# Performance work log

Hardware: AMD Instinct MI355X
Metric: run time of the kernel (lower is better)

## Reference

```python
import jax, jax.numpy as jnp
import numpy as np

N_HEAD = 12

def setup_inputs() -> dict:
    key = jax.random.key(0)
    ks = jax.random.split(key, 5)
    B, T, C = 1, 4096, 768
    scale = 0.02
    return {
        "x": jax.random.normal(ks[0], (B, T, C), jnp.float32),
        "w_attn": jax.random.normal(ks[1], (C, 3 * C), jnp.float32) * scale,
        "b_attn": jax.random.normal(ks[2], (3 * C,), jnp.float32) * scale,
        "w_proj": jax.random.normal(ks[3], (C, C), jnp.float32) * scale,
        "b_proj": jax.random.normal(ks[4], (C,), jnp.float32) * scale,
    }

def reference(x, w_attn, b_attn, w_proj, b_proj):
    B, T, C = x.shape
    H = N_HEAD
    D = C // H
    qkv = x @ w_attn + b_attn                      # [B,T,3C]
    q, k, v = jnp.split(qkv, 3, axis=-1)
    # [B,T,C] -> [B,H,T,D]
    q = q.reshape(B, T, H, D).transpose(0, 2, 1, 3)
    k = k.reshape(B, T, H, D).transpose(0, 2, 1, 3)
    v = v.reshape(B, T, H, D).transpose(0, 2, 1, 3)
    att = jnp.einsum("bhqd,bhkd->bhqk", q, k) * (1.0 / np.sqrt(D))
    causal = jnp.tril(jnp.ones((T, T), bool))
    att = jnp.where(causal[None, None], att, -jnp.inf)
    att = jax.nn.softmax(att, axis=-1)
    y = jnp.einsum("bhqk,bhkd->bhqd", att, v)      # [B,H,T,D]
    y = y.transpose(0, 2, 1, 3).reshape(B, T, C)
    return y @ w_proj + b_proj
```

## Files before the change

### kernel.cpp

```cpp
#include <hip/hip_runtime.h>
#include <hip/hip_bf16.h>
#include <cstdint>
#include <cstddef>

#define NHEAD 12
#define TSEQ  4096
#define CDIM  768

typedef __attribute__((ext_vector_type(8))) short bf16x8;
typedef __attribute__((ext_vector_type(4))) float f32x4;
typedef __attribute__((ext_vector_type(16))) float f32x16;
typedef __attribute__((ext_vector_type(2))) unsigned int u32x2;

typedef __attribute__((address_space(1))) void gvoid;
typedef __attribute__((address_space(3))) void lvoid;

#define QSCALE 0.1803368801111204f

static __device__ __forceinline__ unsigned short f2bf(float f) {
    union { float f; uint32_t u; } v; v.f = f;
    uint32_t u = v.u;
    u += 0x7fffu + ((u >> 16) & 1u);
    return (unsigned short)(u >> 16);
}

static __device__ __forceinline__ f32x4 mfma16(bf16x8 a, bf16x8 b, f32x4 c) {
    return __builtin_amdgcn_mfma_f32_16x16x32_bf16(a, b, c, 0, 0, 0);
}
static __device__ __forceinline__ f32x16 mfma32(bf16x8 a, bf16x8 b, f32x16 c) {
    return __builtin_amdgcn_mfma_f32_32x32x16_bf16(a, b, c, 0, 0, 0);
}
static __device__ __forceinline__ unsigned cvt_pk_bf16(float lo, float hi) {
    unsigned r;
    asm("v_cvt_pk_bf16_f32 %0, %1, %2" : "=v"(r) : "v"(lo), "v"(hi));
    return r;
}


__global__ void cvt_f32_bf16(const float* __restrict__ in, unsigned short* __restrict__ out, int n4) {
    int i = blockIdx.x * blockDim.x + threadIdx.x;
    int stride = gridDim.x * blockDim.x;
    for (int idx = i; idx < n4; idx += stride) {
        float4 v = reinterpret_cast<const float4*>(in)[idx];
        ushort4 o;
        o.x = f2bf(v.x); o.y = f2bf(v.y); o.z = f2bf(v.z); o.w = f2bf(v.w);
        reinterpret_cast<ushort4*>(out)[idx] = o;
    }
}

__global__ void transpose_cvt(const float* __restrict__ W, unsigned short* __restrict__ Wt,
                              int K, int N) {
    __shared__ float tile[32][33];
    int n0 = blockIdx.x * 32;
    int k0 = blockIdx.y * 32;
    int tx = threadIdx.x & 31;
    int ty = threadIdx.x >> 5;
    #pragma unroll
    for (int r = ty; r < 32; r += 8)
        tile[r][tx] = W[(size_t)(k0 + r) * N + n0 + tx];
    __syncthreads();
    #pragma unroll
    for (int r = ty; r < 32; r += 8)
        Wt[(size_t)(n0 + r) * K + k0 + tx] = f2bf(tile[tx][r]);
}


template<int MODE>
__global__ __launch_bounds__(256)
void gemm_bt(const unsigned short* __restrict__ A,
             const unsigned short* __restrict__ Bt,
             const float* __restrict__ bias,
             unsigned short* __restrict__ Qb,
             unsigned short* __restrict__ Kb,
             unsigned short* __restrict__ Vt,
             float* __restrict__ Out,
             int M, int N, int K)
{
    __shared__ __align__(16) unsigned short As[128 * 32];
    __shared__ __align__(16) unsigned short Bs[128 * 32];

    const int tid  = threadIdx.x;
    const int lane = tid & 63;
    const int w    = tid >> 6;
    const int wr   = w >> 1, wc = w & 1;
    const int row0 = blockIdx.x * 128;
    const int col0 = blockIdx.y * 128;
    const int l16  = lane & 15;
    const int lhi  = lane >> 4;

    f32x4 acc[4][4] = {};

    for (int k0 = 0; k0 < K; k0 += 32) {
        __syncthreads();
        #pragma unroll
        for (int r = 0; r < 2; ++r) {
            int b    = r * 4096 + w * 1024 + lane * 16;
            int trow = b >> 6;
            int koff = b & 63;
            const char* gA = (const char*)A  + ((size_t)(row0 + trow) * K + k0) * 2 + koff;
            const char* gB = (const char*)Bt + ((size_t)(col0 + trow) * K + k0) * 2 + koff;
            __builtin_amdgcn_global_load_lds((gvoid*)gA,
                (lvoid*)((char*)As + r * 4096 + w * 1024), 16, 0, 0);
            __builtin_amdgcn_global_load_lds((gvoid*)gB,
                (lvoid*)((char*)Bs + r * 4096 + w * 1024), 16, 0, 0);
        }
        __syncthreads();

        bf16x8 a[4], bfr[4];
        #pragma unroll
        for (int m = 0; m < 4; ++m) {
            int row = wr * 64 + m * 16 + l16;
            a[m] = *reinterpret_cast<const bf16x8*>(&As[row * 32 + lhi * 8]);
        }
        #pragma unroll
        for (int n = 0; n < 4; ++n) {
            int col = wc * 64 + n * 16 + l16;
            bfr[n] = *reinterpret_cast<const bf16x8*>(&Bs[col * 32 + lhi * 8]);
        }
        #pragma unroll
        for (int m = 0; m < 4; ++m)
            #pragma unroll
            for (int n = 0; n < 4; ++n)
                acc[m][n] = mfma16(a[m], bfr[n], acc[m][n]);
    }

    #pragma unroll
    for (int m = 0; m < 4; ++m) {
        int trow = row0 + wr * 64 + m * 16 + lhi * 4;
        #pragma unroll
        for (int n = 0; n < 4; ++n) {
            int ncol = col0 + wc * 64 + n * 16 + l16;
            float bv = bias[ncol];
            #pragma unroll
            for (int j = 0; j < 4; ++j) {
                float v = acc[m][n][j] + bv;
                int t = trow + j;
                if (MODE == 0) {
                    if (ncol < 768) {
                        int hh = ncol >> 6, d = ncol & 63;
                        Qb[((size_t)hh * TSEQ + t) * 64 + d] = f2bf(v * QSCALE);
                    } else if (ncol < 1536) {
                        int c = ncol - 768; int hh = c >> 6, d = c & 63;
                        Kb[((size_t)hh * TSEQ + t) * 64 + d] = f2bf(v);
                    } else {
                        int c = ncol - 1536; int hh = c >> 6, d = c & 63;
                        Vt[((size_t)hh * 64 + d) * TSEQ + t] = f2bf(v);
                    }
                } else {
                    Out[(size_t)t * N + ncol] = v;
                }
            }
        }
    }
}


__global__ __launch_bounds__(64)
void attn_fwd(const unsigned short* __restrict__ Qb,
              const unsigned short* __restrict__ Kb,
              const unsigned short* __restrict__ Vt,
              unsigned short* __restrict__ Y)
{
    const int lane = threadIdx.x & 63;
    const int l31  = lane & 31;
    const int hi   = lane >> 5;
    const int bid  = blockIdx.x;
    const int h    = bid % NHEAD;
    const int qb   = 127 - bid / NHEAD;
    const int q0   = qb * 32;
    const int ntiles = q0 / 64 + 1;

    const unsigned short* Qh = Qb + (size_t)h * TSEQ * 64;
    const unsigned short* Kh = Kb + (size_t)h * TSEQ * 64;
    const unsigned short* Vh = Vt + (size_t)h * 64 * TSEQ;

    bf16x8 qf[4];
    #pragma unroll
    for (int ks = 0; ks < 4; ++ks)
        qf[ks] = *reinterpret_cast<const bf16x8*>(
            &Qh[(size_t)(q0 + l31) * 64 + ks * 16 + hi * 8]);

    f32x16 o0 = {}, o1 = {};
    float mrun = -1e30f, lrun = 0.f;

    bf16x8 kfA[2][4], kfB[2][4];
    #pragma unroll
    for (int sub = 0; sub < 2; ++sub)
        #pragma unroll
        for (int ks = 0; ks < 4; ++ks)
            kfA[sub][ks] = *reinterpret_cast<const bf16x8*>(
                &Kh[(size_t)(sub * 32 + l31) * 64 + ks * 16 + hi * 8]);

    auto body = [&](int kt, bf16x8 (&kc)[2][4], bf16x8 (&kn)[2][4]) {
        const int kv0 = kt * 64;

        bf16x8 vf[2][4];
        #pragma unroll
        for (int d = 0; d < 2; ++d)
            #pragma unroll
            for (int ks = 0; ks < 4; ++ks)
                vf[d][ks] = *reinterpret_cast<const bf16x8*>(
                    &Vh[(size_t)(d * 32 + l31) * TSEQ + kv0 + ks * 16 + hi * 8]);

        f32x16 s0 = {}, s1 = {};
        #pragma unroll
        for (int ks = 0; ks < 4; ++ks) {
            s0 = mfma32(kc[0][ks], qf[ks], s0);
            s1 = mfma32(kc[1][ks], qf[ks], s1);
        }

        if (kt + 1 < ntiles) {
            const int nv0 = kv0 + 64;
            #pragma unroll
            for (int sub = 0; sub < 2; ++sub)
                #pragma unroll
                for (int ks = 0; ks < 4; ++ks)
                    kn[sub][ks] = *reinterpret_cast<const bf16x8*>(
                        &Kh[(size_t)(nv0 + sub * 32 + l31) * 64 + ks * 16 + hi * 8]);
        }

        float sv[32];
        #pragma unroll
        for (int i = 0; i < 16; ++i) { sv[i] = s0[i]; sv[16 + i] = s1[i]; }

        if (kt == ntiles - 1) {
            const int qrel = q0 + l31 - kv0;
            const int h4 = hi * 4;
            #pragma unroll
            for (int i = 0; i < 32; ++i) {
                int kvbase = (i >> 4) * 32 + (i & 3) + 8 * ((i >> 2) & 3);
                if (kvbase + h4 > qrel) sv[i] = -1e30f;
            }
        }

        float t[16];
        #pragma unroll
        for (int i = 0; i < 16; ++i) t[i] = fmaxf(sv[i], sv[i + 16]);
        #pragma unroll
        for (int s = 8; s >= 1; s >>= 1)
            #pragma unroll
            for (int i = 0; i < s; ++i) t[i] = fmaxf(t[i], t[i + s]);
        float mx;
        {
            union { float f; unsigned u; } c; c.f = t[0];
            u32x2 r = __builtin_amdgcn_permlane32_swap(c.u, c.u, false, false);
            union { unsigned u; float f; } ra, rb; ra.u = r.x; rb.u = r.y;
            mx = fmaxf(ra.f, rb.f);
        }
        float mnew = fmaxf(mrun, mx);
        float corr = exp2f(mrun - mnew);
        mrun = mnew;

        float e[32];
        #pragma unroll
        for (int i = 0; i < 32; ++i) e[i] = exp2f(sv[i] - mnew);

        float u[16];
        #pragma unroll
        for (int i = 0; i < 16; ++i) u[i] = e[i] + e[i + 16];
        #pragma unroll
        for (int s = 8; s >= 1; s >>= 1)
            #pragma unroll
            for (int i = 0; i < s; ++i) u[i] += u[i + s];
        float ps;
        {
            union { float f; unsigned u; } c; c.f = u[0];
            u32x2 r = __builtin_amdgcn_permlane32_swap(c.u, c.u, false, false);
            union { unsigned u; float f; } ra, rb; ra.u = r.x; rb.u = r.y;
            ps = ra.f + rb.f;
        }
        lrun = lrun * corr + ps;

        #pragma unroll
        for (int i = 0; i < 16; ++i) { o0[i] *= corr; o1[i] *= corr; }

        bf16x8 pw[4];
        #pragma unroll
        for (int ks = 0; ks < 4; ++ks) {
            const int eb = (ks >> 1) * 16 + (ks & 1) * 8;
            u32x2 r02 = __builtin_amdgcn_permlane32_swap(
                cvt_pk_bf16(e[eb + 0], e[eb + 1]), cvt_pk_bf16(e[eb + 4], e[eb + 5]),
                false, false);
            u32x2 r13 = __builtin_amdgcn_permlane32_swap(
                cvt_pk_bf16(e[eb + 2], e[eb + 3]), cvt_pk_bf16(e[eb + 6], e[eb + 7]),
                false, false);
            union { unsigned w[4]; bf16x8 v; } pk;
            pk.w[0] = r02.x; pk.w[1] = r13.x; pk.w[2] = r02.y; pk.w[3] = r13.y;
            pw[ks] = pk.v;
        }

        #pragma unroll
        for (int ks = 0; ks < 4; ++ks) {
            o0 = mfma32(vf[0][ks], pw[ks], o0);
            o1 = mfma32(vf[1][ks], pw[ks], o1);
        }
    };

    int kt = 0;
    for (; kt + 2 <= ntiles; kt += 2) {
        body(kt, kfA, kfB);
        body(kt + 1, kfB, kfA);
    }
    if (kt < ntiles) body(kt, kfA, kfB);

    float inv = 1.0f / lrun;
    const int trow = q0 + l31;
    #pragma unroll
    for (int d = 0; d < 2; ++d) {
        #pragma unroll
        for (int p = 0; p < 8; ++p) {
            const int rr = p * 2;
            float v0 = (d ? o1 : o0)[rr] * inv;
            float v1 = (d ? o1 : o0)[rr + 1] * inv;
            int c = h * 64 + d * 32 + (rr & 3) + 8 * (rr >> 2) + hi * 4;
            unsigned wd = cvt_pk_bf16(v0, v1);
            *reinterpret_cast<unsigned*>(
                const_cast<unsigned short*>(&Y[(size_t)trow * CDIM + c])) = wd;
        }
    }
}


extern "C" void kernel_launch(void* const* d_in, const int* in_sizes, int n_in,
                              void* d_out, int out_size, void* d_ws, size_t ws_size,
                              hipStream_t stream) {
    const float* x      = (const float*)d_in[0];
    const float* w_attn = (const float*)d_in[1];
    const float* b_attn = (const float*)d_in[2];
    const float* w_proj = (const float*)d_in[3];
    const float* b_proj = (const float*)d_in[4];
    float* out = (float*)d_out;

    char* ws = (char*)d_ws;
    unsigned short* xb  = (unsigned short*)(ws + 0);
    unsigned short* WaT = (unsigned short*)(ws + 6291456);
    unsigned short* WpT = (unsigned short*)(ws + 9830400);
    unsigned short* Qb  = (unsigned short*)(ws + 11010048);
    unsigned short* Kb  = (unsigned short*)(ws + 17301504);
    unsigned short* Vt  = (unsigned short*)(ws + 23592960);
    unsigned short* Yb  = (unsigned short*)(ws + 29884416);

    cvt_f32_bf16<<<2048, 256, 0, stream>>>(x, xb, TSEQ * CDIM / 4);
    transpose_cvt<<<dim3(2304 / 32, 768 / 32), 256, 0, stream>>>(w_attn, WaT, 768, 2304);
    transpose_cvt<<<dim3(768 / 32, 768 / 32), 256, 0, stream>>>(w_proj, WpT, 768, 768);

    gemm_bt<0><<<dim3(TSEQ / 128, 2304 / 128), 256, 0, stream>>>(
        xb, WaT, b_attn, Qb, Kb, Vt, nullptr, TSEQ, 2304, CDIM);

    attn_fwd<<<NHEAD * (TSEQ / 32), 64, 0, stream>>>(Qb, Kb, Vt, Yb);

    gemm_bt<1><<<dim3(TSEQ / 128, CDIM / 128), 256, 0, stream>>>(
        Yb, WpT, b_proj, nullptr, nullptr, nullptr, out, TSEQ, CDIM, CDIM);
}
```

Before: 250.8 us.

## Split attention KV tiles across four waves per block with shared-memory merge

Each attention block now runs four waves, and each wave processes every fourth KV tile for the same 32-query strip. The partial outputs, running maxima and sums from waves 1-3 go through shared memory and are merged by wave 0 with rescaling. This targets the long serial KV loop of the single-wave design and the imbalance between causal blocks. In exchange it drops the register double-buffered K prefetch, adds about 25KB of LDS per block plus a barrier, and leaves waves idle on short rows.

Result: slower. 292.0 us (+16.4%).

```diff
diff --git a/kernel.cpp b/kernel.cpp
--- a/kernel.cpp
+++ b/kernel.cpp
@@ -155,13 +155,19 @@
 }
 
 
-__global__ __launch_bounds__(64)
+__global__ __launch_bounds__(256, 4)
 void attn_fwd(const unsigned short* __restrict__ Qb,
               const unsigned short* __restrict__ Kb,
               const unsigned short* __restrict__ Vt,
               unsigned short* __restrict__ Y)
 {
-    const int lane = threadIdx.x & 63;
+    __shared__ __align__(16) float Osh[3][32][64];
+    __shared__ float Msh[3][64];
+    __shared__ float Lsh[3][64];
+
+    const int tid  = threadIdx.x;
+    const int lane = tid & 63;
+    const int w    = tid >> 6;
     const int l31  = lane & 31;
     const int hi   = lane >> 5;
     const int bid  = blockIdx.x;
@@ -183,16 +189,16 @@
     f32x16 o0 = {}, o1 = {};
     float mrun = -1e30f, lrun = 0.f;
 
-    bf16x8 kfA[2][4], kfB[2][4];
-    #pragma unroll
-    for (int sub = 0; sub < 2; ++sub)
-        #pragma unroll
-        for (int ks = 0; ks < 4; ++ks)
-            kfA[sub][ks] = *reinterpret_cast<const bf16x8*>(
-                &Kh[(size_t)(sub * 32 + l31) * 64 + ks * 16 + hi * 8]);
-
-    auto body = [&](int kt, bf16x8 (&kc)[2][4], bf16x8 (&kn)[2][4]) {
+    for (int kt = w; kt < ntiles; kt += 4) {
         const int kv0 = kt * 64;
+
+        bf16x8 kf[2][4];
+        #pragma unroll
+        for (int sub = 0; sub < 2; ++sub)
+            #pragma unroll
+            for (int ks = 0; ks < 4; ++ks)
+                kf[sub][ks] = *reinterpret_cast<const bf16x8*>(
+                    &Kh[(size_t)(kv0 + sub * 32 + l31) * 64 + ks * 16 + hi * 8]);
 
         bf16x8 vf[2][4];
         #pragma unroll
@@ -205,18 +211,8 @@
         f32x16 s0 = {}, s1 = {};
         #pragma unroll
         for (int ks = 0; ks < 4; ++ks) {
-            s0 = mfma32(kc[0][ks], qf[ks], s0);
-            s1 = mfma32(kc[1][ks], qf[ks], s1);
-        }
-
-        if (kt + 1 < ntiles) {
-            const int nv0 = kv0 + 64;
-            #pragma unroll
-            for (int sub = 0; sub < 2; ++sub)
-                #pragma unroll
-                for (int ks = 0; ks < 4; ++ks)
-                    kn[sub][ks] = *reinterpret_cast<const bf16x8*>(
-                        &Kh[(size_t)(nv0 + sub * 32 + l31) * 64 + ks * 16 + hi * 8]);
+            s0 = mfma32(kf[0][ks], qf[ks], s0);
+            s1 = mfma32(kf[1][ks], qf[ks], s1);
         }
 
         float sv[32];
@@ -284,8 +280,8 @@
             u32x2 r13 = __builtin_amdgcn_permlane32_swap(
                 cvt_pk_bf16(e[eb + 2], e[eb + 3]), cvt_pk_bf16(e[eb + 6], e[eb + 7]),
                 false, false);
-            union { unsigned w[4]; bf16x8 v; } pk;
-            pk.w[0] = r02.x; pk.w[1] = r13.x; pk.w[2] = r02.y; pk.w[3] = r13.y;
+            union { unsigned wd[4]; bf16x8 v; } pk;
+            pk.wd[0] = r02.x; pk.wd[1] = r13.x; pk.wd[2] = r02.y; pk.wd[3] = r13.y;
             pw[ks] = pk.v;
         }
 
@@ -294,28 +290,47 @@
             o0 = mfma32(vf[0][ks], pw[ks], o0);
             o1 = mfma32(vf[1][ks], pw[ks], o1);
         }
-    };
-
-    int kt = 0;
-    for (; kt + 2 <= ntiles; kt += 2) {
-        body(kt, kfA, kfB);
-        body(kt + 1, kfB, kfA);
-    }
-    if (kt < ntiles) body(kt, kfA, kfB);
-
-    float inv = 1.0f / lrun;
-    const int trow = q0 + l31;
-    #pragma unroll
-    for (int d = 0; d < 2; ++d) {
-        #pragma unroll
-        for (int p = 0; p < 8; ++p) {
-            const int rr = p * 2;
-            float v0 = (d ? o1 : o0)[rr] * inv;
-            float v1 = (d ? o1 : o0)[rr + 1] * inv;
-            int c = h * 64 + d * 32 + (rr & 3) + 8 * (rr >> 2) + hi * 4;
-            unsigned wd = cvt_pk_bf16(v0, v1);
-            *reinterpret_cast<unsigned*>(
-                const_cast<unsigned short*>(&Y[(size_t)trow * CDIM + c])) = wd;
+    }
+
+    if (w > 0) {
+        #pragma unroll
+        for (int i = 0; i < 16; ++i) {
+            Osh[w - 1][i][lane]      = o0[i];
+            Osh[w - 1][16 + i][lane] = o1[i];
+        }
+        Msh[w - 1][lane] = mrun;
+        Lsh[w - 1][lane] = lrun;
+    }
+    __syncthreads();
+    if (w == 0) {
+        #pragma unroll
+        for (int p = 0; p < 3; ++p) {
+            float mp = Msh[p][lane], lp = Lsh[p][lane];
+            float mn = fmaxf(mrun, mp);
+            float a = exp2f(mrun - mn), b = exp2f(mp - mn);
+            #pragma unroll
+            for (int i = 0; i < 16; ++i) {
+                o0[i] = o0[i] * a + Osh[p][i][lane] * b;
+                o1[i] = o1[i] * a + Osh[p][16 + i][lane] * b;
+            }
+            lrun = lrun * a + lp * b;
+            mrun = mn;
+        }
+
+        float inv = 1.0f / lrun;
+        const int trow = q0 + l31;
+        #pragma unroll
+        for (int d = 0; d < 2; ++d) {
+            #pragma unroll
+            for (int p = 0; p < 8; ++p) {
+                const int rr = p * 2;
+                float v0 = (d ? o1 : o0)[rr] * inv;
+                float v1 = (d ? o1 : o0)[rr + 1] * inv;
+                int c = h * 64 + d * 32 + (rr & 3) + 8 * (rr >> 2) + hi * 4;
+                unsigned wd = cvt_pk_bf16(v0, v1);
+                *reinterpret_cast<unsigned*>(
+                    const_cast<unsigned short*>(&Y[(size_t)trow * CDIM + c])) = wd;
+            }
         }
     }
 }
@@ -347,7 +362,7 @@
     gemm_bt<0><<<dim3(TSEQ / 128, 2304 / 128), 256, 0, stream>>>(
         xb, WaT, b_attn, Qb, Kb, Vt, nullptr, TSEQ, 2304, CDIM);
 
-    attn_fwd<<<NHEAD * (TSEQ / 32), 64, 0, stream>>>(Qb, Kb, Vt, Yb);
+    attn_fwd<<<NHEAD * (TSEQ / 32), 256, 0, stream>>>(Qb, Kb, Vt, Yb);
 
     gemm_bt<1><<<dim3(TSEQ / 128, CDIM / 128), 256, 0, stream>>>(
         Yb, WpT, b_proj, nullptr, nullptr, nullptr, out, TSEQ, CDIM, CDIM);
```
